# Kernel optimization log

Hardware: AMD Instinct MI355X
Metric: run time of the kernel (lower is better)

The kernel has to match this reference:

```python
import jax, jax.numpy as jnp
import numpy as np

B, T, D, H, W = 256, 512, 64, 128, 256

def _init_linear(key, out_dim, in_dim):
    lim = 1.0 / np.sqrt(in_dim)
    return jax.random.uniform(key, (out_dim, in_dim), jnp.float32, -lim, lim)

def setup_inputs():
    key = jax.random.key(0)
    ks = jax.random.split(key, 12)
    inp = {}
    inp['ts'] = jnp.arange(T, dtype=jnp.float32)
    for n, k in zip(['coeffs_d', 'coeffs_c', 'coeffs_b', 'coeffs_a'], ks[:4]):
        inp[n] = jax.random.normal(k, (B, T - 1, D), jnp.float32) * 0.05
    # initial MLP: D -> W -> W -> H (relu hidden, identity final)
    inp['i_w0'] = _init_linear(ks[4], W, D); inp['i_b0'] = jnp.zeros((W,), jnp.float32)
    inp['i_w1'] = _init_linear(ks[5], W, W); inp['i_b1'] = jnp.zeros((W,), jnp.float32)
    inp['i_w2'] = _init_linear(ks[6], H, W); inp['i_b2'] = jnp.zeros((H,), jnp.float32)
    # func MLP: H -> W -> W -> H*D (softplus hidden, tanh final)
    inp['f_w0'] = _init_linear(ks[7], W, H); inp['f_b0'] = jnp.zeros((W,), jnp.float32)
    inp['f_w1'] = _init_linear(ks[8], W, W); inp['f_b1'] = jnp.zeros((W,), jnp.float32)
    inp['f_w2'] = _init_linear(ks[9], H * D, W); inp['f_b2'] = jnp.zeros((H * D,), jnp.float32)
    # readout linear: H -> 1
    inp['l_w'] = _init_linear(ks[10], 1, H); inp['l_b'] = jnp.zeros((1,), jnp.float32)
    return inp

def reference(ts, coeffs_d, coeffs_c, coeffs_b, coeffs_a,
              i_w0, i_b0, i_w1, i_b1, i_w2, i_b2,
              f_w0, f_b0, f_w1, f_b1, f_w2, f_b2,
              l_w, l_b):
    dt = ts[1] - ts[0]
    # cubic spline value at t=ts[0]: interval 0, frac 0 -> a[0]
    x0 = coeffs_a[:, 0, :]  # [B, D]
    h = jax.nn.relu(x0 @ i_w0.T + i_b0)
    h = jax.nn.relu(h @ i_w1.T + i_b1)
    y0 = h @ i_w2.T + i_b2  # [B, H]

    def step(carry, _):
        t, y = carry
        # cubic spline derivative at t: b + 2c*frac + 3d*frac^2 on interval idx
        idx = jnp.clip(jnp.searchsorted(ts, t, side='right') - 1, 0, T - 2)
        frac = t - ts[idx]
        deriv = coeffs_b[:, idx] + 2.0 * coeffs_c[:, idx] * frac + 3.0 * coeffs_d[:, idx] * (frac * frac)  # [B, D]
        # vector field f(y): [B, H, D]
        g = jax.nn.softplus(y @ f_w0.T + f_b0)
        g = jax.nn.softplus(g @ f_w1.T + f_b1)
        f = jnp.tanh(g @ f_w2.T + f_b2).reshape(B, H, D)
        # Euler step: y1 = y + (f @ dX/dt) * dt
        y1 = y + jnp.einsum('bhd,bd->bh', f, deriv) * dt
        return (t + dt, y1), y1

    _, ys = jax.lax.scan(step, (ts[0], y0), None, length=T)
    # prediction = sigmoid(linear(ys[-1]))[0], per batch element
    return jax.nn.sigmoid(ys[-1] @ l_w.T + l_b)[:, 0]  # [B]
```

## Files before the change

kernel.cpp:

```cpp
#include <hip/hip_runtime.h>
#include <hip/hip_bf16.h>
#include <stdint.h>


#define BB 256
#define DD 64
#define HH 128
#define WW 256
#define HD 8192
#define TSTEPS 512
#define PAD_Y 152
#define PAD_G 280
#define PAD_DV 68

typedef __bf16 bf16x8 __attribute__((ext_vector_type(8)));
typedef __bf16 bf16x4 __attribute__((ext_vector_type(4)));
typedef float f32x4 __attribute__((ext_vector_type(4)));

__device__ __forceinline__ float softplus_f(float x) {
  return (x > 15.f) ? x : __logf(1.f + __expf(x));
}
__device__ __forceinline__ float tanh_f(float x) {
  float e = __expf(2.f * x);
  return 1.f - 2.f / (e + 1.f);
}

__device__ __forceinline__ void publish_y(uint32_t* slot, int idx, float val, uint32_t tag) {
  unsigned short ub = __builtin_bit_cast(unsigned short, (__bf16)val);
  __hip_atomic_store(&slot[idx], (tag << 16) | (uint32_t)ub,
                     __ATOMIC_RELAXED, __HIP_MEMORY_SCOPE_AGENT);
}

__global__ void prep_kernel(const float* __restrict__ w0, const float* __restrict__ w1,
                            const float* __restrict__ w2,
                            __bf16* __restrict__ w0b, __bf16* __restrict__ w1b,
                            __bf16* __restrict__ w2b) {
  int stride = gridDim.x * blockDim.x;
  int i0 = blockIdx.x * blockDim.x + threadIdx.x;
  for (int i = i0; i < WW * HH; i += stride) w0b[i] = (__bf16)w0[i];
  for (int i = i0; i < WW * WW; i += stride) w1b[i] = (__bf16)w1[i];
  for (int i = i0; i < HD * WW; i += stride) w2b[i] = (__bf16)w2[i];
}

__global__ __launch_bounds__(256) void init_kernel(
    const float* __restrict__ ca, const float* __restrict__ iw0, const float* __restrict__ ib0,
    const float* __restrict__ iw1, const float* __restrict__ ib1,
    const float* __restrict__ iw2, const float* __restrict__ ib2,
    float* __restrict__ y0) {
  __shared__ float x0[DD];
  __shared__ float h0[WW];
  __shared__ float h1[WW];
  int b = blockIdx.x, t = threadIdx.x;
  if (t < DD) x0[t] = ca[((size_t)b * 511) * DD + t];
  __syncthreads();
  float a = ib0[t];
  for (int d = 0; d < DD; ++d) a = fmaf(x0[d], iw0[t * DD + d], a);
  h0[t] = fmaxf(a, 0.f);
  __syncthreads();
  a = ib1[t];
  for (int d = 0; d < WW; ++d) a = fmaf(h0[d], iw1[t * WW + d], a);
  h1[t] = fmaxf(a, 0.f);
  __syncthreads();
  if (t < HH) {
    a = ib2[t];
    for (int d = 0; d < WW; ++d) a = fmaf(h1[d], iw2[t * WW + d], a);
    y0[b * HH + t] = a;
  }
}

__global__ __launch_bounds__(512, 2) void step_persist(
    const __bf16* __restrict__ w0b, const __bf16* __restrict__ w1b, const __bf16* __restrict__ w2b,
    const float* __restrict__ fb0, const float* __restrict__ fb1, const float* __restrict__ fb2,
    const float* __restrict__ cbp, const float* __restrict__ ccp, const float* __restrict__ cdp,
    float* __restrict__ yA, uint32_t* __restrict__ pk)
{
  __shared__ __align__(16) __bf16 yb[32 * PAD_Y];
  __shared__ __align__(16) __bf16 g0s[32 * PAD_G];
  __shared__ __align__(16) __bf16 g1s[32 * PAD_G];
  __shared__ __align__(16) float dv[32 * PAD_DV];
  __shared__ float pbuf[8 * 32];

  const int tid = threadIdx.x;
  const int wv = tid >> 6;
  const int l = tid & 63;
  const int l16 = l & 15;
  const int lq = l >> 4;

  const int wid = blockIdx.x;
  const int grp = wid >> 5;
  const int j = wid & 31;
  const int rb = grp * 32;
  const int c0 = j * 256;

  bf16x8 w0f[4][2], w1f[8][2], w2f[8][2];
  #pragma unroll
  for (int c = 0; c < 2; ++c) {
    int col = wv * 32 + c * 16 + l16;
    #pragma unroll
    for (int kb = 0; kb < 4; ++kb)
      w0f[kb][c] = *(const bf16x8*)&w0b[col * HH + kb * 32 + lq * 8];
    #pragma unroll
    for (int kb = 0; kb < 8; ++kb)
      w1f[kb][c] = *(const bf16x8*)&w1b[col * WW + kb * 32 + lq * 8];
    #pragma unroll
    for (int kb = 0; kb < 8; ++kb)
      w2f[kb][c] = *(const bf16x8*)&w2b[(size_t)(c0 + col) * WW + kb * 32 + lq * 8];
  }
  f32x4 b0r[2], b1r[2], b2r[2];
  #pragma unroll
  for (int c = 0; c < 2; ++c) {
    b0r[c] = *(const f32x4*)&fb0[wv * 32 + c * 16 + lq * 4];
    b1r[c] = *(const f32x4*)&fb1[wv * 32 + c * 16 + lq * 4];
    b2r[c] = *(const f32x4*)&fb2[c0 + wv * 32 + c * 16 + lq * 4];
  }

  float yreg = 0.f;
  int myidx = 0;
  if (tid < 128) {
    int r = tid & 31, hl = tid >> 5;
    myidx = (rb + r) * HH + (4 * j + hl);
    yreg = yA[myidx];
    publish_y(pk, myidx, yreg, 1u);
  }

  for (int k = 0; k < TSTEPS; ++k) {
    const uint32_t want = (uint32_t)(k + 1);
    const uint32_t* src = pk + (size_t)(k & 1) * (BB * HH);

    float dreg[4];
    {
      int kk = (k <= 510) ? k : 510;
      #pragma unroll
      for (int q = 0; q < 4; ++q) {
        int i = tid + q * 512;
        int r = i >> 6, d = i & (DD - 1);
        int off = ((rb + r) * 511 + kk) * DD + d;
        float v = cbp[off];
        if (k == 511) v += 2.f * ccp[off] + 3.f * cdp[off];
        dreg[q] = v;
      }
    }

    {
      uint32_t v[8];
      int ad[8];
      #pragma unroll
      for (int q = 0; q < 8; ++q) {
        int i = tid + q * 512;
        ad[q] = (rb + (i >> 7)) * HH + (i & (HH - 1));
        v[q] = __hip_atomic_load(&src[ad[q]], __ATOMIC_RELAXED, __HIP_MEMORY_SCOPE_AGENT);
      }
      int spins = 0;
      bool allok;
      do {
        allok = true;
        #pragma unroll
        for (int q = 0; q < 8; ++q) {
          if ((v[q] >> 16) != want) {
            allok = false;
            v[q] = __hip_atomic_load(&src[ad[q]], __ATOMIC_RELAXED, __HIP_MEMORY_SCOPE_AGENT);
          }
        }
        if (!allok) {
          __builtin_amdgcn_s_sleep(1);
          if (++spins > (1 << 20)) break;
        }
      } while (!allok);
      #pragma unroll
      for (int q = 0; q < 8; ++q) {
        int i = tid + q * 512;
        yb[(i >> 7) * PAD_Y + (i & (HH - 1))] =
            __builtin_bit_cast(__bf16, (unsigned short)(v[q] & 0xFFFFu));
      }
    }
    __syncthreads();

    {
      f32x4 acc[2][2] = {};
      #pragma unroll
      for (int kb = 0; kb < 4; ++kb) {
        bf16x8 y0 = *(const bf16x8*)&yb[l16 * PAD_Y + kb * 32 + lq * 8];
        bf16x8 y1 = *(const bf16x8*)&yb[(16 + l16) * PAD_Y + kb * 32 + lq * 8];
        #pragma unroll
        for (int c = 0; c < 2; ++c) {
          acc[c][0] = __builtin_amdgcn_mfma_f32_16x16x32_bf16(w0f[kb][c], y0, acc[c][0], 0, 0, 0);
          acc[c][1] = __builtin_amdgcn_mfma_f32_16x16x32_bf16(w0f[kb][c], y1, acc[c][1], 0, 0, 0);
        }
      }
      #pragma unroll
      for (int c = 0; c < 2; ++c)
        #pragma unroll
        for (int bt = 0; bt < 2; ++bt) {
          bf16x4 o;
          #pragma unroll
          for (int r = 0; r < 4; ++r)
            o[r] = (__bf16)softplus_f(acc[c][bt][r] + b0r[c][r]);
          *(bf16x4*)&g0s[(bt * 16 + l16) * PAD_G + wv * 32 + c * 16 + lq * 4] = o;
        }
    }
    #pragma unroll
    for (int q = 0; q < 4; ++q) {
      int i = tid + q * 512;
      dv[(i >> 6) * PAD_DV + (i & (DD - 1))] = dreg[q];
    }
    __syncthreads();

    {
      f32x4 acc[2][2] = {};
      #pragma unroll
      for (int kb = 0; kb < 8; ++kb) {
        bf16x8 a0 = *(const bf16x8*)&g0s[l16 * PAD_G + kb * 32 + lq * 8];
        bf16x8 a1 = *(const bf16x8*)&g0s[(16 + l16) * PAD_G + kb * 32 + lq * 8];
        #pragma unroll
        for (int c = 0; c < 2; ++c) {
          acc[c][0] = __builtin_amdgcn_mfma_f32_16x16x32_bf16(w1f[kb][c], a0, acc[c][0], 0, 0, 0);
          acc[c][1] = __builtin_amdgcn_mfma_f32_16x16x32_bf16(w1f[kb][c], a1, acc[c][1], 0, 0, 0);
        }
      }
      #pragma unroll
      for (int c = 0; c < 2; ++c)
        #pragma unroll
        for (int bt = 0; bt < 2; ++bt) {
          bf16x4 o;
          #pragma unroll
          for (int r = 0; r < 4; ++r)
            o[r] = (__bf16)softplus_f(acc[c][bt][r] + b1r[c][r]);
          *(bf16x4*)&g1s[(bt * 16 + l16) * PAD_G + wv * 32 + c * 16 + lq * 4] = o;
        }
    }
    __syncthreads();

    {
      f32x4 acc[2][2] = {};
      #pragma unroll
      for (int kb = 0; kb < 8; ++kb) {
        bf16x8 a0 = *(const bf16x8*)&g1s[l16 * PAD_G + kb * 32 + lq * 8];
        bf16x8 a1 = *(const bf16x8*)&g1s[(16 + l16) * PAD_G + kb * 32 + lq * 8];
        #pragma unroll
        for (int c = 0; c < 2; ++c) {
          acc[c][0] = __builtin_amdgcn_mfma_f32_16x16x32_bf16(w2f[kb][c], a0, acc[c][0], 0, 0, 0);
          acc[c][1] = __builtin_amdgcn_mfma_f32_16x16x32_bf16(w2f[kb][c], a1, acc[c][1], 0, 0, 0);
        }
      }
      #pragma unroll
      for (int bt = 0; bt < 2; ++bt) {
        float p = 0.f;
        #pragma unroll
        for (int c = 0; c < 2; ++c) {
          f32x4 dvv = *(const f32x4*)&dv[(bt * 16 + l16) * PAD_DV +
                                         (wv & 1) * 32 + c * 16 + lq * 4];
          #pragma unroll
          for (int r = 0; r < 4; ++r) {
            float f = tanh_f(acc[c][bt][r] + b2r[c][r]);
            p = fmaf(f, dvv[r], p);
          }
        }
        p += __shfl_xor(p, 16);
        p += __shfl_xor(p, 32);
        if (l < 16) pbuf[wv * 32 + bt * 16 + l] = p;
      }
    }
    __syncthreads();

    if (tid < 128) {
      int hl = tid >> 5, r = tid & 31;
      yreg += pbuf[(2 * hl) * 32 + r] + pbuf[(2 * hl + 1) * 32 + r];
      publish_y(pk + (size_t)((k + 1) & 1) * (BB * HH), myidx, yreg, (uint32_t)(k + 2));
    }
    __syncthreads();
  }

  if (tid < 128) yA[myidx] = yreg;
}

__global__ __launch_bounds__(256) void final_kernel(const float* __restrict__ y,
                                                    const float* __restrict__ lw,
                                                    const float* __restrict__ lb,
                                                    float* __restrict__ out) {
  int b = threadIdx.x;
  float a = lb[0];
  for (int h = 0; h < HH; ++h) a = fmaf(y[b * HH + h], lw[h], a);
  out[b] = 1.f / (1.f + __expf(-a));
}

extern "C" void kernel_launch(void* const* d_in, const int* in_sizes, int n_in,
                              void* d_out, int out_size, void* d_ws, size_t ws_size,
                              hipStream_t stream) {
  const float* cdp = (const float*)d_in[1];
  const float* ccp = (const float*)d_in[2];
  const float* cbp = (const float*)d_in[3];
  const float* cap = (const float*)d_in[4];
  const float* iw0 = (const float*)d_in[5];
  const float* ib0 = (const float*)d_in[6];
  const float* iw1 = (const float*)d_in[7];
  const float* ib1 = (const float*)d_in[8];
  const float* iw2 = (const float*)d_in[9];
  const float* ib2 = (const float*)d_in[10];
  const float* fw0 = (const float*)d_in[11];
  const float* fb0 = (const float*)d_in[12];
  const float* fw1 = (const float*)d_in[13];
  const float* fb1 = (const float*)d_in[14];
  const float* fw2 = (const float*)d_in[15];
  const float* fb2 = (const float*)d_in[16];
  const float* lw  = (const float*)d_in[17];
  const float* lb  = (const float*)d_in[18];

  char* ws = (char*)d_ws;
  __bf16* w0b = (__bf16*)(ws);
  __bf16* w1b = (__bf16*)(ws + 65536);
  __bf16* w2b = (__bf16*)(ws + 65536 + 131072);
  float* yA = (float*)(ws + 65536 + 131072 + 4194304);
  uint32_t* pk = (uint32_t*)(ws + 65536 + 131072 + 4194304 + 131072);

  hipMemsetAsync(pk, 0, 2 * BB * HH * sizeof(uint32_t), stream);
  prep_kernel<<<512, 256, 0, stream>>>(fw0, fw1, fw2, w0b, w1b, w2b);
  init_kernel<<<BB, 256, 0, stream>>>(cap, iw0, ib0, iw1, ib1, iw2, ib2, yA);
  step_persist<<<256, 512, 0, stream>>>(w0b, w1b, w2b, fb0, fb1, fb2,
                                        cbp, ccp, cdp, yA, pk);
  final_kernel<<<1, 256, 0, stream>>>(yA, lw, lb, (float*)d_out);

  (void)in_sizes; (void)n_in; (void)out_size; (void)ws_size;
}
```

Measured before the change: 4.053 ms.

## Split first two MLP layers onto two leader blocks per group with flag sync

Previously every one of the 32 blocks in a batch group recomputed the first two MLP layers for all 32 rows. Now two leader blocks per group each compute those layers for 16 rows, publish the second hidden activation to global memory, and signal through a per-group flag. All blocks then spin on the flags, load the shared activations and run the large third layer. Per-element tagged y values are replaced by plain float stores plus per-block flags, and spline pointers are advanced incrementally. The intent is to remove redundant layer-1/2 work and cut polling traffic. The cost is an extra global handoff and dependency on the leaders on the critical path every step, and occupancy is lowered to one block per CU.

```diff
diff --git a/kernel.cpp b/kernel.cpp
--- a/kernel.cpp
+++ b/kernel.cpp
@@ -9,6 +9,8 @@
 #define WW 256
 #define HD 8192
 #define TSTEPS 512
+#define NGRP 8
+#define GSZ 32
 #define PAD_Y 152
 #define PAD_G 280
 #define PAD_DV 68
@@ -24,11 +26,16 @@
   float e = __expf(2.f * x);
   return 1.f - 2.f / (e + 1.f);
 }
-
-__device__ __forceinline__ void publish_y(uint32_t* slot, int idx, float val, uint32_t tag) {
-  unsigned short ub = __builtin_bit_cast(unsigned short, (__bf16)val);
-  __hip_atomic_store(&slot[idx], (tag << 16) | (uint32_t)ub,
-                     __ATOMIC_RELAXED, __HIP_MEMORY_SCOPE_AGENT);
+__device__ __forceinline__ uint32_t pack_bf16x2(float a, float b) {
+  unsigned short ua = __builtin_bit_cast(unsigned short, (__bf16)a);
+  unsigned short ub = __builtin_bit_cast(unsigned short, (__bf16)b);
+  return (uint32_t)ua | ((uint32_t)ub << 16);
+}
+__device__ __forceinline__ uint32_t aload(const uint32_t* p) {
+  return __hip_atomic_load(p, __ATOMIC_RELAXED, __HIP_MEMORY_SCOPE_AGENT);
+}
+__device__ __forceinline__ void astore(uint32_t* p, uint32_t v) {
+  __hip_atomic_store(p, v, __ATOMIC_RELAXED, __HIP_MEMORY_SCOPE_AGENT);
 }
 
 __global__ void prep_kernel(const float* __restrict__ w0, const float* __restrict__ w1,
@@ -68,14 +75,15 @@
   }
 }
 
-__global__ __launch_bounds__(512, 2) void step_persist(
+__global__ __launch_bounds__(512, 1) void step_persist(
     const __bf16* __restrict__ w0b, const __bf16* __restrict__ w1b, const __bf16* __restrict__ w2b,
     const float* __restrict__ fb0, const float* __restrict__ fb1, const float* __restrict__ fb2,
     const float* __restrict__ cbp, const float* __restrict__ ccp, const float* __restrict__ cdp,
-    float* __restrict__ yA, uint32_t* __restrict__ pk)
+    float* __restrict__ yA, uint32_t* __restrict__ pky, uint32_t* __restrict__ pg,
+    uint32_t* __restrict__ yflag, uint32_t* __restrict__ gflag)
 {
-  __shared__ __align__(16) __bf16 yb[32 * PAD_Y];
-  __shared__ __align__(16) __bf16 g0s[32 * PAD_G];
+  __shared__ __align__(16) __bf16 yb[16 * PAD_Y];
+  __shared__ __align__(16) __bf16 g0s[16 * PAD_G];
   __shared__ __align__(16) __bf16 g1s[32 * PAD_G];
   __shared__ __align__(16) float dv[32 * PAD_DV];
   __shared__ float pbuf[8 * 32];
@@ -89,29 +97,31 @@
   const int wid = blockIdx.x;
   const int grp = wid >> 5;
   const int j = wid & 31;
+  const int jr = (j - 4 * grp) & 31;
+  const bool isLeader = (jr < 2);
   const int rb = grp * 32;
   const int c0 = j * 256;
 
-  bf16x8 w0f[4][2], w1f[8][2], w2f[8][2];
+  bf16x8 w2f[8][2];
+  f32x4 b2r[2];
   #pragma unroll
   for (int c = 0; c < 2; ++c) {
     int col = wv * 32 + c * 16 + l16;
     #pragma unroll
-    for (int kb = 0; kb < 4; ++kb)
-      w0f[kb][c] = *(const bf16x8*)&w0b[col * HH + kb * 32 + lq * 8];
-    #pragma unroll
-    for (int kb = 0; kb < 8; ++kb)
-      w1f[kb][c] = *(const bf16x8*)&w1b[col * WW + kb * 32 + lq * 8];
-    #pragma unroll
     for (int kb = 0; kb < 8; ++kb)
       w2f[kb][c] = *(const bf16x8*)&w2b[(size_t)(c0 + col) * WW + kb * 32 + lq * 8];
-  }
-  f32x4 b0r[2], b1r[2], b2r[2];
+    b2r[c] = *(const f32x4*)&fb2[c0 + wv * 32 + c * 16 + lq * 4];
+  }
+
+  const float* pcb[4];
+  float ex[4];
   #pragma unroll
-  for (int c = 0; c < 2; ++c) {
-    b0r[c] = *(const f32x4*)&fb0[wv * 32 + c * 16 + lq * 4];
-    b1r[c] = *(const f32x4*)&fb1[wv * 32 + c * 16 + lq * 4];
-    b2r[c] = *(const f32x4*)&fb2[c0 + wv * 32 + c * 16 + lq * 4];
+  for (int q = 0; q < 4; ++q) {
+    int i = tid + q * 512;
+    int r = i >> 6, d = i & (DD - 1);
+    size_t base = ((size_t)(rb + r) * 511) * DD + d;
+    pcb[q] = cbp + base;
+    ex[q] = 2.f * ccp[base + (size_t)510 * DD] + 3.f * cdp[base + (size_t)510 * DD];
   }
 
   float yreg = 0.f;
@@ -120,113 +130,125 @@
     int r = tid & 31, hl = tid >> 5;
     myidx = (rb + r) * HH + (4 * j + hl);
     yreg = yA[myidx];
-    publish_y(pk, myidx, yreg, 1u);
-  }
+    astore(&pky[myidx], __builtin_bit_cast(uint32_t, yreg));
+  }
+  __syncthreads();
+  if (tid == 0) astore(&yflag[grp * GSZ + j], 1u);
 
   for (int k = 0; k < TSTEPS; ++k) {
     const uint32_t want = (uint32_t)(k + 1);
-    const uint32_t* src = pk + (size_t)(k & 1) * (BB * HH);
-
-    float dreg[4];
-    {
-      int kk = (k <= 510) ? k : 510;
+
+    #pragma unroll
+    for (int q = 0; q < 4; ++q) {
+      float v = *pcb[q];
+      if (k < 510) pcb[q] += DD;
+      if (k == 511) v += ex[q];
+      int i = tid + q * 512;
+      dv[(i >> 6) * PAD_DV + (i & (DD - 1))] = v;
+    }
+
+    uint32_t* pgs = pg + (size_t)(k & 1) * (NGRP * 4096) + grp * 4096;
+
+    if (isLeader) {
+      bf16x8 w0t[4][2], w1t[8][2];
+      f32x4 b0r[2], b1r[2];
       #pragma unroll
-      for (int q = 0; q < 4; ++q) {
-        int i = tid + q * 512;
-        int r = i >> 6, d = i & (DD - 1);
-        int off = ((rb + r) * 511 + kk) * DD + d;
-        float v = cbp[off];
-        if (k == 511) v += 2.f * ccp[off] + 3.f * cdp[off];
-        dreg[q] = v;
-      }
-    }
-
-    {
-      uint32_t v[8];
-      int ad[8];
-      #pragma unroll
-      for (int q = 0; q < 8; ++q) {
-        int i = tid + q * 512;
-        ad[q] = (rb + (i >> 7)) * HH + (i & (HH - 1));
-        v[q] = __hip_atomic_load(&src[ad[q]], __ATOMIC_RELAXED, __HIP_MEMORY_SCOPE_AGENT);
-      }
-      int spins = 0;
-      bool allok;
-      do {
-        allok = true;
-        #pragma unroll
-        for (int q = 0; q < 8; ++q) {
-          if ((v[q] >> 16) != want) {
-            allok = false;
-            v[q] = __hip_atomic_load(&src[ad[q]], __ATOMIC_RELAXED, __HIP_MEMORY_SCOPE_AGENT);
-          }
-        }
-        if (!allok) {
+      for (int c = 0; c < 2; ++c) {
+        int col = wv * 32 + c * 16 + l16;
+        #pragma unroll
+        for (int kb = 0; kb < 4; ++kb)
+          w0t[kb][c] = *(const bf16x8*)&w0b[col * HH + kb * 32 + lq * 8];
+        #pragma unroll
+        for (int kb = 0; kb < 8; ++kb)
+          w1t[kb][c] = *(const bf16x8*)&w1b[col * WW + kb * 32 + lq * 8];
+        b0r[c] = *(const f32x4*)&fb0[wv * 32 + c * 16 + lq * 4];
+        b1r[c] = *(const f32x4*)&fb1[wv * 32 + c * 16 + lq * 4];
+      }
+      {
+        const uint32_t* yf = yflag + grp * GSZ + (l & 31);
+        const bool need = (l < 32);
+        int spins = 0;
+        while (true) {
+          uint32_t f = need ? aload(yf) : want;
+          if (__all(f == want)) break;
           __builtin_amdgcn_s_sleep(1);
-          if (++spins > (1 << 20)) break;
-        }
-      } while (!allok);
-      #pragma unroll
-      for (int q = 0; q < 8; ++q) {
-        int i = tid + q * 512;
-        yb[(i >> 7) * PAD_Y + (i & (HH - 1))] =
-            __builtin_bit_cast(__bf16, (unsigned short)(v[q] & 0xFFFFu));
-      }
-    }
-    __syncthreads();
-
-    {
-      f32x4 acc[2][2] = {};
-      #pragma unroll
-      for (int kb = 0; kb < 4; ++kb) {
-        bf16x8 y0 = *(const bf16x8*)&yb[l16 * PAD_Y + kb * 32 + lq * 8];
-        bf16x8 y1 = *(const bf16x8*)&yb[(16 + l16) * PAD_Y + kb * 32 + lq * 8];
+          if (++spins > (1 << 22)) break;
+        }
+      }
+      __asm__ __volatile__("" ::: "memory");
+      {
+        const uint32_t* ysl = pky + (size_t)(k & 1) * (BB * HH);
+        #pragma unroll
+        for (int q = 0; q < 4; ++q) {
+          int i = tid + q * 512;
+          int rl = i >> 7, h = i & (HH - 1);
+          uint32_t w = aload(&ysl[(rb + 16 * jr + rl) * HH + h]);
+          yb[rl * PAD_Y + h] = (__bf16)__builtin_bit_cast(float, w);
+        }
+      }
+      __syncthreads();
+      {
+        f32x4 acc[2] = {};
+        #pragma unroll
+        for (int kb = 0; kb < 4; ++kb) {
+          bf16x8 yf8 = *(const bf16x8*)&yb[l16 * PAD_Y + kb * 32 + lq * 8];
+          #pragma unroll
+          for (int c = 0; c < 2; ++c)
+            acc[c] = __builtin_amdgcn_mfma_f32_16x16x32_bf16(w0t[kb][c], yf8, acc[c], 0, 0, 0);
+        }
         #pragma unroll
         for (int c = 0; c < 2; ++c) {
-          acc[c][0] = __builtin_amdgcn_mfma_f32_16x16x32_bf16(w0f[kb][c], y0, acc[c][0], 0, 0, 0);
-          acc[c][1] = __builtin_amdgcn_mfma_f32_16x16x32_bf16(w0f[kb][c], y1, acc[c][1], 0, 0, 0);
-        }
-      }
-      #pragma unroll
-      for (int c = 0; c < 2; ++c)
-        #pragma unroll
-        for (int bt = 0; bt < 2; ++bt) {
           bf16x4 o;
           #pragma unroll
           for (int r = 0; r < 4; ++r)
-            o[r] = (__bf16)softplus_f(acc[c][bt][r] + b0r[c][r]);
-          *(bf16x4*)&g0s[(bt * 16 + l16) * PAD_G + wv * 32 + c * 16 + lq * 4] = o;
-        }
-    }
+            o[r] = (__bf16)softplus_f(acc[c][r] + b0r[c][r]);
+          *(bf16x4*)&g0s[l16 * PAD_G + wv * 32 + c * 16 + lq * 4] = o;
+        }
+      }
+      __syncthreads();
+      {
+        f32x4 acc[2] = {};
+        #pragma unroll
+        for (int kb = 0; kb < 8; ++kb) {
+          bf16x8 a8 = *(const bf16x8*)&g0s[l16 * PAD_G + kb * 32 + lq * 8];
+          #pragma unroll
+          for (int c = 0; c < 2; ++c)
+            acc[c] = __builtin_amdgcn_mfma_f32_16x16x32_bf16(w1t[kb][c], a8, acc[c], 0, 0, 0);
+        }
+        int gr = 16 * jr + l16;
+        #pragma unroll
+        for (int c = 0; c < 2; ++c) {
+          float v0 = softplus_f(acc[c][0] + b1r[c][0]);
+          float v1 = softplus_f(acc[c][1] + b1r[c][1]);
+          float v2 = softplus_f(acc[c][2] + b1r[c][2]);
+          float v3 = softplus_f(acc[c][3] + b1r[c][3]);
+          int p = wv * 16 + c * 8 + lq * 2;
+          astore(&pgs[gr * 128 + p], pack_bf16x2(v0, v1));
+          astore(&pgs[gr * 128 + p + 1], pack_bf16x2(v2, v3));
+        }
+      }
+      __syncthreads();
+      if (tid == 0) astore(&gflag[grp * 2 + jr], want);
+    }
+
+    {
+      const uint32_t* gf = gflag + grp * 2 + (l & 1);
+      const bool need = (l < 2);
+      int spins = 0;
+      while (true) {
+        uint32_t f = need ? aload(gf) : want;
+        if (__all(f == want)) break;
+        __builtin_amdgcn_s_sleep(2);
+        if (++spins > (1 << 22)) break;
+      }
+    }
+    __asm__ __volatile__("" ::: "memory");
     #pragma unroll
-    for (int q = 0; q < 4; ++q) {
+    for (int q = 0; q < 8; ++q) {
       int i = tid + q * 512;
-      dv[(i >> 6) * PAD_DV + (i & (DD - 1))] = dreg[q];
-    }
-    __syncthreads();
-
-    {
-      f32x4 acc[2][2] = {};
-      #pragma unroll
-      for (int kb = 0; kb < 8; ++kb) {
-        bf16x8 a0 = *(const bf16x8*)&g0s[l16 * PAD_G + kb * 32 + lq * 8];
-        bf16x8 a1 = *(const bf16x8*)&g0s[(16 + l16) * PAD_G + kb * 32 + lq * 8];
-        #pragma unroll
-        for (int c = 0; c < 2; ++c) {
-          acc[c][0] = __builtin_amdgcn_mfma_f32_16x16x32_bf16(w1f[kb][c], a0, acc[c][0], 0, 0, 0);
-          acc[c][1] = __builtin_amdgcn_mfma_f32_16x16x32_bf16(w1f[kb][c], a1, acc[c][1], 0, 0, 0);
-        }
-      }
-      #pragma unroll
-      for (int c = 0; c < 2; ++c)
-        #pragma unroll
-        for (int bt = 0; bt < 2; ++bt) {
-          bf16x4 o;
-          #pragma unroll
-          for (int r = 0; r < 4; ++r)
-            o[r] = (__bf16)softplus_f(acc[c][bt][r] + b1r[c][r]);
-          *(bf16x4*)&g1s[(bt * 16 + l16) * PAD_G + wv * 32 + c * 16 + lq * 4] = o;
-        }
+      int row = i >> 7, p = i & 127;
+      uint32_t w = aload(&pgs[row * 128 + p]);
+      *(uint32_t*)&g1s[row * PAD_G + 2 * p] = w;
     }
     __syncthreads();
 
@@ -265,9 +287,11 @@
     if (tid < 128) {
       int hl = tid >> 5, r = tid & 31;
       yreg += pbuf[(2 * hl) * 32 + r] + pbuf[(2 * hl + 1) * 32 + r];
-      publish_y(pk + (size_t)((k + 1) & 1) * (BB * HH), myidx, yreg, (uint32_t)(k + 2));
+      uint32_t* ydst = pky + (size_t)((k + 1) & 1) * (BB * HH);
+      astore(&ydst[myidx], __builtin_bit_cast(uint32_t, yreg));
     }
     __syncthreads();
+    if (tid == 0) astore(&yflag[grp * GSZ + j], (uint32_t)(k + 2));
   }
 
   if (tid < 128) yA[myidx] = yreg;
@@ -308,15 +332,18 @@
   char* ws = (char*)d_ws;
   __bf16* w0b = (__bf16*)(ws);
   __bf16* w1b = (__bf16*)(ws + 65536);
-  __bf16* w2b = (__bf16*)(ws + 65536 + 131072);
-  float* yA = (float*)(ws + 65536 + 131072 + 4194304);
-  uint32_t* pk = (uint32_t*)(ws + 65536 + 131072 + 4194304 + 131072);
-
-  hipMemsetAsync(pk, 0, 2 * BB * HH * sizeof(uint32_t), stream);
+  __bf16* w2b = (__bf16*)(ws + 196608);
+  float* yA = (float*)(ws + 4390912);
+  uint32_t* pky = (uint32_t*)(ws + 4521984);
+  uint32_t* pg  = (uint32_t*)(ws + 4784128);
+  uint32_t* yflag = (uint32_t*)(ws + 5046272);
+  uint32_t* gflag = (uint32_t*)(ws + 5047296);
+
+  hipMemsetAsync(yflag, 0, 2048, stream);
   prep_kernel<<<512, 256, 0, stream>>>(fw0, fw1, fw2, w0b, w1b, w2b);
   init_kernel<<<BB, 256, 0, stream>>>(cap, iw0, ib0, iw1, ib1, iw2, ib2, yA);
   step_persist<<<256, 512, 0, stream>>>(w0b, w1b, w2b, fb0, fb1, fb2,
-                                        cbp, ccp, cdp, yA, pk);
+                                        cbp, ccp, cdp, yA, pky, pg, yflag, gflag);
   final_kernel<<<1, 256, 0, stream>>>(yA, lw, lb, (float*)d_out);
 
   (void)in_sizes; (void)n_in; (void)out_size; (void)ws_size;
```

New measurement: 7.615 ms. +87.9%, slower.

## Move W2 weights to LDS, reload W0/W1 per step, load spline derivs directly

Applied to the files above, without the earlier changes.

The per-block W2 weight slice moves from registers into dynamic LDS (about 158 KB), and W0/W1 fragments are re-fetched from global/L2 each time step instead of being held in registers. This cuts register pressure. The g0/g1 buffers are merged into one reused buffer, which adds barriers between the layers. Spline derivative values are now loaded straight into MFMA-layout registers instead of being staged through LDS. The trade-off is more LDS and L2 traffic per step and extra synchronisation, in exchange for fewer VGPRs and possibly less spilling.

```diff
diff --git a/kernel.cpp b/kernel.cpp
--- a/kernel.cpp
+++ b/kernel.cpp
@@ -9,9 +9,14 @@
 #define WW 256
 #define HD 8192
 #define TSTEPS 512
-#define PAD_Y 152
-#define PAD_G 280
-#define PAD_DV 68
+#define PAD_Y 136
+#define PAD_G 264
+
+#define SM_W2   0
+#define SM_YB   131072
+#define SM_G    140288
+#define SM_PBUF 157184
+#define SM_TOT  158208
 
 typedef __bf16 bf16x8 __attribute__((ext_vector_type(8)));
 typedef __bf16 bf16x4 __attribute__((ext_vector_type(4)));
@@ -24,7 +29,6 @@
   float e = __expf(2.f * x);
   return 1.f - 2.f / (e + 1.f);
 }
-
 __device__ __forceinline__ void publish_y(uint32_t* slot, int idx, float val, uint32_t tag) {
   unsigned short ub = __builtin_bit_cast(unsigned short, (__bf16)val);
   __hip_atomic_store(&slot[idx], (tag << 16) | (uint32_t)ub,
@@ -68,17 +72,18 @@
   }
 }
 
-__global__ __launch_bounds__(512, 2) void step_persist(
+__global__ __attribute__((amdgpu_flat_work_group_size(512, 512), amdgpu_waves_per_eu(2, 2)))
+void step_persist(
     const __bf16* __restrict__ w0b, const __bf16* __restrict__ w1b, const __bf16* __restrict__ w2b,
     const float* __restrict__ fb0, const float* __restrict__ fb1, const float* __restrict__ fb2,
     const float* __restrict__ cbp, const float* __restrict__ ccp, const float* __restrict__ cdp,
     float* __restrict__ yA, uint32_t* __restrict__ pk)
 {
-  __shared__ __align__(16) __bf16 yb[32 * PAD_Y];
-  __shared__ __align__(16) __bf16 g0s[32 * PAD_G];
-  __shared__ __align__(16) __bf16 g1s[32 * PAD_G];
-  __shared__ __align__(16) float dv[32 * PAD_DV];
-  __shared__ float pbuf[8 * 32];
+  extern __shared__ __align__(16) char smem[];
+  __bf16* w2l = (__bf16*)(smem + SM_W2);
+  __bf16* yb  = (__bf16*)(smem + SM_YB);
+  __bf16* g   = (__bf16*)(smem + SM_G);
+  float* pbuf = (float*)(smem + SM_PBUF);
 
   const int tid = threadIdx.x;
   const int wv = tid >> 6;
@@ -92,20 +97,13 @@
   const int rb = grp * 32;
   const int c0 = j * 256;
 
-  bf16x8 w0f[4][2], w1f[8][2], w2f[8][2];
-  #pragma unroll
-  for (int c = 0; c < 2; ++c) {
-    int col = wv * 32 + c * 16 + l16;
-    #pragma unroll
-    for (int kb = 0; kb < 4; ++kb)
-      w0f[kb][c] = *(const bf16x8*)&w0b[col * HH + kb * 32 + lq * 8];
-    #pragma unroll
-    for (int kb = 0; kb < 8; ++kb)
-      w1f[kb][c] = *(const bf16x8*)&w1b[col * WW + kb * 32 + lq * 8];
-    #pragma unroll
-    for (int kb = 0; kb < 8; ++kb)
-      w2f[kb][c] = *(const bf16x8*)&w2b[(size_t)(c0 + col) * WW + kb * 32 + lq * 8];
-  }
+  for (int blk = tid; blk < 8192; blk += 512) {
+    int kq = blk >> 8, col = blk & 255;
+    int kb = kq >> 2, lq2 = kq & 3;
+    *(bf16x8*)&w2l[(size_t)blk * 8] =
+        *(const bf16x8*)&w2b[(size_t)(c0 + col) * WW + kb * 32 + lq2 * 8];
+  }
+
   f32x4 b0r[2], b1r[2], b2r[2];
   #pragma unroll
   for (int c = 0; c < 2; ++c) {
@@ -113,6 +111,13 @@
     b1r[c] = *(const f32x4*)&fb1[wv * 32 + c * 16 + lq * 4];
     b2r[c] = *(const f32x4*)&fb2[c0 + wv * 32 + c * 16 + lq * 4];
   }
+
+  size_t cb2[2];
+  #pragma unroll
+  for (int bt = 0; bt < 2; ++bt)
+    cb2[bt] = ((size_t)(rb + bt * 16 + l16) * 511) * DD + (wv & 1) * 32 + lq * 4;
+
+  const int w2base = lq * 2048 + (wv * 32 + l16) * 8;
 
   float yreg = 0.f;
   int myidx = 0;
@@ -122,24 +127,24 @@
     yreg = yA[myidx];
     publish_y(pk, myidx, yreg, 1u);
   }
+  __syncthreads();
 
   for (int k = 0; k < TSTEPS; ++k) {
     const uint32_t want = (uint32_t)(k + 1);
     const uint32_t* src = pk + (size_t)(k & 1) * (BB * HH);
 
-    float dreg[4];
-    {
-      int kk = (k <= 510) ? k : 510;
-      #pragma unroll
-      for (int q = 0; q < 4; ++q) {
-        int i = tid + q * 512;
-        int r = i >> 6, d = i & (DD - 1);
-        int off = ((rb + r) * 511 + kk) * DD + d;
-        float v = cbp[off];
-        if (k == 511) v += 2.f * ccp[off] + 3.f * cdp[off];
-        dreg[q] = v;
-      }
-    }
+    bf16x8 w0f[4][2], w1f[8][2];
+    #pragma unroll
+    for (int c = 0; c < 2; ++c) {
+      int col = wv * 32 + c * 16 + l16;
+      #pragma unroll
+      for (int kb = 0; kb < 4; ++kb)
+        w0f[kb][c] = *(const bf16x8*)&w0b[col * HH + kb * 32 + lq * 8];
+      #pragma unroll
+      for (int kb = 0; kb < 8; ++kb)
+        w1f[kb][c] = *(const bf16x8*)&w1b[col * WW + kb * 32 + lq * 8];
+    }
+    __asm__ __volatile__("" ::: "memory");
 
     {
       uint32_t v[8];
@@ -195,51 +200,68 @@
           #pragma unroll
           for (int r = 0; r < 4; ++r)
             o[r] = (__bf16)softplus_f(acc[c][bt][r] + b0r[c][r]);
-          *(bf16x4*)&g0s[(bt * 16 + l16) * PAD_G + wv * 32 + c * 16 + lq * 4] = o;
-        }
-    }
+          *(bf16x4*)&g[(bt * 16 + l16) * PAD_G + wv * 32 + c * 16 + lq * 4] = o;
+        }
+    }
+    __syncthreads();
+
+    f32x4 dv_[2][2];
+    {
+      size_t ko = (size_t)((k <= 510) ? k : 510) * DD;
+      #pragma unroll
+      for (int bt = 0; bt < 2; ++bt)
+        #pragma unroll
+        for (int c = 0; c < 2; ++c) {
+          size_t off = cb2[bt] + ko + c * 16;
+          dv_[bt][c] = *(const f32x4*)&cbp[off];
+          if (k == 511) {
+            f32x4 cc = *(const f32x4*)&ccp[off];
+            f32x4 dd = *(const f32x4*)&cdp[off];
+            #pragma unroll
+            for (int r = 0; r < 4; ++r)
+              dv_[bt][c][r] += 2.f * cc[r] + 3.f * dd[r];
+          }
+        }
+    }
+
+    f32x4 acc1[2][2] = {};
+    {
+      #pragma unroll
+      for (int kb = 0; kb < 8; ++kb) {
+        bf16x8 a0 = *(const bf16x8*)&g[l16 * PAD_G + kb * 32 + lq * 8];
+        bf16x8 a1 = *(const bf16x8*)&g[(16 + l16) * PAD_G + kb * 32 + lq * 8];
+        #pragma unroll
+        for (int c = 0; c < 2; ++c) {
+          acc1[c][0] = __builtin_amdgcn_mfma_f32_16x16x32_bf16(w1f[kb][c], a0, acc1[c][0], 0, 0, 0);
+          acc1[c][1] = __builtin_amdgcn_mfma_f32_16x16x32_bf16(w1f[kb][c], a1, acc1[c][1], 0, 0, 0);
+        }
+      }
+    }
+    __syncthreads();
+
     #pragma unroll
-    for (int q = 0; q < 4; ++q) {
-      int i = tid + q * 512;
-      dv[(i >> 6) * PAD_DV + (i & (DD - 1))] = dreg[q];
-    }
+    for (int c = 0; c < 2; ++c)
+      #pragma unroll
+      for (int bt = 0; bt < 2; ++bt) {
+        bf16x4 o;
+        #pragma unroll
+        for (int r = 0; r < 4; ++r)
+          o[r] = (__bf16)softplus_f(acc1[c][bt][r] + b1r[c][r]);
+        *(bf16x4*)&g[(bt * 16 + l16) * PAD_G + wv * 32 + c * 16 + lq * 4] = o;
+      }
     __syncthreads();
 
     {
       f32x4 acc[2][2] = {};
       #pragma unroll
       for (int kb = 0; kb < 8; ++kb) {
-        bf16x8 a0 = *(const bf16x8*)&g0s[l16 * PAD_G + kb * 32 + lq * 8];
-        bf16x8 a1 = *(const bf16x8*)&g0s[(16 + l16) * PAD_G + kb * 32 + lq * 8];
-        #pragma unroll
-        for (int c = 0; c < 2; ++c) {
-          acc[c][0] = __builtin_amdgcn_mfma_f32_16x16x32_bf16(w1f[kb][c], a0, acc[c][0], 0, 0, 0);
-          acc[c][1] = __builtin_amdgcn_mfma_f32_16x16x32_bf16(w1f[kb][c], a1, acc[c][1], 0, 0, 0);
-        }
-      }
-      #pragma unroll
-      for (int c = 0; c < 2; ++c)
-        #pragma unroll
-        for (int bt = 0; bt < 2; ++bt) {
-          bf16x4 o;
-          #pragma unroll
-          for (int r = 0; r < 4; ++r)
-            o[r] = (__bf16)softplus_f(acc[c][bt][r] + b1r[c][r]);
-          *(bf16x4*)&g1s[(bt * 16 + l16) * PAD_G + wv * 32 + c * 16 + lq * 4] = o;
-        }
-    }
-    __syncthreads();
-
-    {
-      f32x4 acc[2][2] = {};
-      #pragma unroll
-      for (int kb = 0; kb < 8; ++kb) {
-        bf16x8 a0 = *(const bf16x8*)&g1s[l16 * PAD_G + kb * 32 + lq * 8];
-        bf16x8 a1 = *(const bf16x8*)&g1s[(16 + l16) * PAD_G + kb * 32 + lq * 8];
-        #pragma unroll
-        for (int c = 0; c < 2; ++c) {
-          acc[c][0] = __builtin_amdgcn_mfma_f32_16x16x32_bf16(w2f[kb][c], a0, acc[c][0], 0, 0, 0);
-          acc[c][1] = __builtin_amdgcn_mfma_f32_16x16x32_bf16(w2f[kb][c], a1, acc[c][1], 0, 0, 0);
+        bf16x8 a0 = *(const bf16x8*)&g[l16 * PAD_G + kb * 32 + lq * 8];
+        bf16x8 a1 = *(const bf16x8*)&g[(16 + l16) * PAD_G + kb * 32 + lq * 8];
+        #pragma unroll
+        for (int c = 0; c < 2; ++c) {
+          bf16x8 wf = *(const bf16x8*)&w2l[w2base + kb * 8192 + c * 128];
+          acc[c][0] = __builtin_amdgcn_mfma_f32_16x16x32_bf16(wf, a0, acc[c][0], 0, 0, 0);
+          acc[c][1] = __builtin_amdgcn_mfma_f32_16x16x32_bf16(wf, a1, acc[c][1], 0, 0, 0);
         }
       }
       #pragma unroll
@@ -247,12 +269,10 @@
         float p = 0.f;
         #pragma unroll
         for (int c = 0; c < 2; ++c) {
-          f32x4 dvv = *(const f32x4*)&dv[(bt * 16 + l16) * PAD_DV +
-                                         (wv & 1) * 32 + c * 16 + lq * 4];
           #pragma unroll
           for (int r = 0; r < 4; ++r) {
             float f = tanh_f(acc[c][bt][r] + b2r[c][r]);
-            p = fmaf(f, dvv[r], p);
+            p = fmaf(f, dv_[bt][c][r], p);
           }
         }
         p += __shfl_xor(p, 16);
@@ -315,8 +335,8 @@
   hipMemsetAsync(pk, 0, 2 * BB * HH * sizeof(uint32_t), stream);
   prep_kernel<<<512, 256, 0, stream>>>(fw0, fw1, fw2, w0b, w1b, w2b);
   init_kernel<<<BB, 256, 0, stream>>>(cap, iw0, ib0, iw1, ib1, iw2, ib2, yA);
-  step_persist<<<256, 512, 0, stream>>>(w0b, w1b, w2b, fb0, fb1, fb2,
-                                        cbp, ccp, cdp, yA, pk);
+  step_persist<<<256, 512, SM_TOT, stream>>>(w0b, w1b, w2b, fb0, fb1, fb2,
+                                             cbp, ccp, cdp, yA, pk);
   final_kernel<<<1, 256, 0, stream>>>(yA, lw, lb, (float*)d_out);
 
   (void)in_sizes; (void)n_in; (void)out_size; (void)ws_size;
```

Result: slower. 4.361 ms (+7.6%).

## Remap final layer per wave to drop shared-memory reduction and barriers

Applied to the files above, without the earlier changes.

The final GEMM is reorganised so each wave owns a 16-row by one-h output tile, covering 64 columns with 4 MFMA accumulators. The dot product with the spline derivative and the Euler update then finish inside the wave and are published directly, which removes the pbuf reduction, the dv staging in shared memory and two block barriers per step. Derivative coefficients are loaded as vectors straight into registers, and the y buffer is double-buffered so the end-of-step barrier can go. The cost is that w2 is no longer held in registers and is reloaded from global memory/L2 on every step, alongside a VGPR cap attribute and smaller padding.

```diff
diff --git a/kernel.cpp b/kernel.cpp
--- a/kernel.cpp
+++ b/kernel.cpp
@@ -9,9 +9,8 @@
 #define WW 256
 #define HD 8192
 #define TSTEPS 512
-#define PAD_Y 152
-#define PAD_G 280
-#define PAD_DV 68
+#define PAD_Y 136
+#define PAD_G 264
 
 typedef __bf16 bf16x8 __attribute__((ext_vector_type(8)));
 typedef __bf16 bf16x4 __attribute__((ext_vector_type(4)));
@@ -24,7 +23,9 @@
   float e = __expf(2.f * x);
   return 1.f - 2.f / (e + 1.f);
 }
-
+__device__ __forceinline__ uint32_t aload(const uint32_t* p) {
+  return __hip_atomic_load(p, __ATOMIC_RELAXED, __HIP_MEMORY_SCOPE_AGENT);
+}
 __device__ __forceinline__ void publish_y(uint32_t* slot, int idx, float val, uint32_t tag) {
   unsigned short ub = __builtin_bit_cast(unsigned short, (__bf16)val);
   __hip_atomic_store(&slot[idx], (tag << 16) | (uint32_t)ub,
@@ -68,17 +69,19 @@
   }
 }
 
-__global__ __launch_bounds__(512, 2) void step_persist(
+__global__ __attribute__((amdgpu_flat_work_group_size(512, 512), amdgpu_waves_per_eu(2, 2)))
+#if __has_attribute(amdgpu_num_vgpr)
+__attribute__((amdgpu_num_vgpr(224)))
+#endif
+void step_persist(
     const __bf16* __restrict__ w0b, const __bf16* __restrict__ w1b, const __bf16* __restrict__ w2b,
     const float* __restrict__ fb0, const float* __restrict__ fb1, const float* __restrict__ fb2,
     const float* __restrict__ cbp, const float* __restrict__ ccp, const float* __restrict__ cdp,
     float* __restrict__ yA, uint32_t* __restrict__ pk)
 {
-  __shared__ __align__(16) __bf16 yb[32 * PAD_Y];
+  __shared__ __align__(16) __bf16 yb[2][32 * PAD_Y];
   __shared__ __align__(16) __bf16 g0s[32 * PAD_G];
   __shared__ __align__(16) __bf16 g1s[32 * PAD_G];
-  __shared__ __align__(16) float dv[32 * PAD_DV];
-  __shared__ float pbuf[8 * 32];
 
   const int tid = threadIdx.x;
   const int wv = tid >> 6;
@@ -91,34 +94,33 @@
   const int j = wid & 31;
   const int rb = grp * 32;
   const int c0 = j * 256;
-
-  bf16x8 w0f[4][2], w1f[8][2], w2f[8][2];
+  const int rt = wv >> 2;
+  const int hq = wv & 3;
+
+  bf16x8 w0f[4][2], w1f[8][2];
+  f32x4 b0r[2], b1r[2];
   #pragma unroll
-  for (int c = 0; c < 2; ++c) {
-    int col = wv * 32 + c * 16 + l16;
+  for (int cc = 0; cc < 2; ++cc) {
+    int colA = wv * 32 + cc * 16 + l16;
     #pragma unroll
     for (int kb = 0; kb < 4; ++kb)
-      w0f[kb][c] = *(const bf16x8*)&w0b[col * HH + kb * 32 + lq * 8];
+      w0f[kb][cc] = *(const bf16x8*)&w0b[colA * HH + kb * 32 + lq * 8];
     #pragma unroll
     for (int kb = 0; kb < 8; ++kb)
-      w1f[kb][c] = *(const bf16x8*)&w1b[col * WW + kb * 32 + lq * 8];
-    #pragma unroll
-    for (int kb = 0; kb < 8; ++kb)
-      w2f[kb][c] = *(const bf16x8*)&w2b[(size_t)(c0 + col) * WW + kb * 32 + lq * 8];
+      w1f[kb][cc] = *(const bf16x8*)&w1b[colA * WW + kb * 32 + lq * 8];
+    b0r[cc] = *(const f32x4*)&fb0[wv * 32 + cc * 16 + lq * 4];
+    b1r[cc] = *(const f32x4*)&fb1[wv * 32 + cc * 16 + lq * 4];
   }
-  f32x4 b0r[2], b1r[2], b2r[2];
+  f32x4 b2r[4];
   #pragma unroll
-  for (int c = 0; c < 2; ++c) {
-    b0r[c] = *(const f32x4*)&fb0[wv * 32 + c * 16 + lq * 4];
-    b1r[c] = *(const f32x4*)&fb1[wv * 32 + c * 16 + lq * 4];
-    b2r[c] = *(const f32x4*)&fb2[c0 + wv * 32 + c * 16 + lq * 4];
-  }
-
+  for (int c = 0; c < 4; ++c)
+    b2r[c] = *(const f32x4*)&fb2[c0 + hq * 64 + c * 16 + lq * 4];
+
+  const size_t dvbase = ((size_t)(rb + rt * 16 + l16) * 511) * DD + lq * 4;
+
+  const int myidx = (rb + rt * 16 + l16) * HH + (4 * j + hq);
   float yreg = 0.f;
-  int myidx = 0;
-  if (tid < 128) {
-    int r = tid & 31, hl = tid >> 5;
-    myidx = (rb + r) * HH + (4 * j + hl);
+  if (l < 16) {
     yreg = yA[myidx];
     publish_y(pk, myidx, yreg, 1u);
   }
@@ -126,18 +128,21 @@
   for (int k = 0; k < TSTEPS; ++k) {
     const uint32_t want = (uint32_t)(k + 1);
     const uint32_t* src = pk + (size_t)(k & 1) * (BB * HH);
-
-    float dreg[4];
-    {
-      int kk = (k <= 510) ? k : 510;
-      #pragma unroll
-      for (int q = 0; q < 4; ++q) {
-        int i = tid + q * 512;
-        int r = i >> 6, d = i & (DD - 1);
-        int off = ((rb + r) * 511 + kk) * DD + d;
-        float v = cbp[off];
-        if (k == 511) v += 2.f * ccp[off] + 3.f * cdp[off];
-        dreg[q] = v;
+    __bf16* ybk = yb[k & 1];
+
+    f32x4 dvv[4];
+    {
+      size_t ko = dvbase + (size_t)((k <= 510) ? k : 510) * DD;
+      #pragma unroll
+      for (int c = 0; c < 4; ++c) dvv[c] = *(const f32x4*)&cbp[ko + c * 16];
+      if (k == 511) {
+        #pragma unroll
+        for (int c = 0; c < 4; ++c) {
+          f32x4 cc = *(const f32x4*)&ccp[ko + c * 16];
+          f32x4 dd = *(const f32x4*)&cdp[ko + c * 16];
+          #pragma unroll
+          for (int r = 0; r < 4; ++r) dvv[c][r] += 2.f * cc[r] + 3.f * dd[r];
+        }
       }
     }
 
@@ -147,8 +152,8 @@
       #pragma unroll
       for (int q = 0; q < 8; ++q) {
         int i = tid + q * 512;
-        ad[q] = (rb + (i >> 7)) * HH + (i & (HH - 1));
-        v[q] = __hip_atomic_load(&src[ad[q]], __ATOMIC_RELAXED, __HIP_MEMORY_SCOPE_AGENT);
+        ad[q] = (rb + (i >> 7)) * HH + (i & 127);
+        v[q] = aload(&src[ad[q]]);
       }
       int spins = 0;
       bool allok;
@@ -158,7 +163,7 @@
         for (int q = 0; q < 8; ++q) {
           if ((v[q] >> 16) != want) {
             allok = false;
-            v[q] = __hip_atomic_load(&src[ad[q]], __ATOMIC_RELAXED, __HIP_MEMORY_SCOPE_AGENT);
+            v[q] = aload(&src[ad[q]]);
           }
         }
         if (!allok) {
@@ -169,7 +174,7 @@
       #pragma unroll
       for (int q = 0; q < 8; ++q) {
         int i = tid + q * 512;
-        yb[(i >> 7) * PAD_Y + (i & (HH - 1))] =
+        ybk[(i >> 7) * PAD_Y + (i & 127)] =
             __builtin_bit_cast(__bf16, (unsigned short)(v[q] & 0xFFFFu));
       }
     }
@@ -179,29 +184,24 @@
       f32x4 acc[2][2] = {};
       #pragma unroll
       for (int kb = 0; kb < 4; ++kb) {
-        bf16x8 y0 = *(const bf16x8*)&yb[l16 * PAD_Y + kb * 32 + lq * 8];
-        bf16x8 y1 = *(const bf16x8*)&yb[(16 + l16) * PAD_Y + kb * 32 + lq * 8];
-        #pragma unroll
-        for (int c = 0; c < 2; ++c) {
-          acc[c][0] = __builtin_amdgcn_mfma_f32_16x16x32_bf16(w0f[kb][c], y0, acc[c][0], 0, 0, 0);
-          acc[c][1] = __builtin_amdgcn_mfma_f32_16x16x32_bf16(w0f[kb][c], y1, acc[c][1], 0, 0, 0);
-        }
-      }
-      #pragma unroll
-      for (int c = 0; c < 2; ++c)
+        bf16x8 y0 = *(const bf16x8*)&ybk[l16 * PAD_Y + kb * 32 + lq * 8];
+        bf16x8 y1 = *(const bf16x8*)&ybk[(16 + l16) * PAD_Y + kb * 32 + lq * 8];
+        #pragma unroll
+        for (int cc = 0; cc < 2; ++cc) {
+          acc[cc][0] = __builtin_amdgcn_mfma_f32_16x16x32_bf16(w0f[kb][cc], y0, acc[cc][0], 0, 0, 0);
+          acc[cc][1] = __builtin_amdgcn_mfma_f32_16x16x32_bf16(w0f[kb][cc], y1, acc[cc][1], 0, 0, 0);
+        }
+      }
+      #pragma unroll
+      for (int cc = 0; cc < 2; ++cc)
         #pragma unroll
         for (int bt = 0; bt < 2; ++bt) {
           bf16x4 o;
           #pragma unroll
           for (int r = 0; r < 4; ++r)
-            o[r] = (__bf16)softplus_f(acc[c][bt][r] + b0r[c][r]);
-          *(bf16x4*)&g0s[(bt * 16 + l16) * PAD_G + wv * 32 + c * 16 + lq * 4] = o;
-        }
-    }
-    #pragma unroll
-    for (int q = 0; q < 4; ++q) {
-      int i = tid + q * 512;
-      dv[(i >> 6) * PAD_DV + (i & (DD - 1))] = dreg[q];
+            o[r] = (__bf16)softplus_f(acc[cc][bt][r] + b0r[cc][r]);
+          *(bf16x4*)&g0s[(bt * 16 + l16) * PAD_G + wv * 32 + cc * 16 + lq * 4] = o;
+        }
     }
     __syncthreads();
 
@@ -212,65 +212,54 @@
         bf16x8 a0 = *(const bf16x8*)&g0s[l16 * PAD_G + kb * 32 + lq * 8];
         bf16x8 a1 = *(const bf16x8*)&g0s[(16 + l16) * PAD_G + kb * 32 + lq * 8];
         #pragma unroll
-        for (int c = 0; c < 2; ++c) {
-          acc[c][0] = __builtin_amdgcn_mfma_f32_16x16x32_bf16(w1f[kb][c], a0, acc[c][0], 0, 0, 0);
-          acc[c][1] = __builtin_amdgcn_mfma_f32_16x16x32_bf16(w1f[kb][c], a1, acc[c][1], 0, 0, 0);
-        }
-      }
-      #pragma unroll
-      for (int c = 0; c < 2; ++c)
+        for (int cc = 0; cc < 2; ++cc) {
+          acc[cc][0] = __builtin_amdgcn_mfma_f32_16x16x32_bf16(w1f[kb][cc], a0, acc[cc][0], 0, 0, 0);
+          acc[cc][1] = __builtin_amdgcn_mfma_f32_16x16x32_bf16(w1f[kb][cc], a1, acc[cc][1], 0, 0, 0);
+        }
+      }
+      #pragma unroll
+      for (int cc = 0; cc < 2; ++cc)
         #pragma unroll
         for (int bt = 0; bt < 2; ++bt) {
           bf16x4 o;
           #pragma unroll
           for (int r = 0; r < 4; ++r)
-            o[r] = (__bf16)softplus_f(acc[c][bt][r] + b1r[c][r]);
-          *(bf16x4*)&g1s[(bt * 16 + l16) * PAD_G + wv * 32 + c * 16 + lq * 4] = o;
+            o[r] = (__bf16)softplus_f(acc[cc][bt][r] + b1r[cc][r]);
+          *(bf16x4*)&g1s[(bt * 16 + l16) * PAD_G + wv * 32 + cc * 16 + lq * 4] = o;
         }
     }
     __syncthreads();
 
     {
-      f32x4 acc[2][2] = {};
+      f32x4 acc[4] = {};
       #pragma unroll
       for (int kb = 0; kb < 8; ++kb) {
-        bf16x8 a0 = *(const bf16x8*)&g1s[l16 * PAD_G + kb * 32 + lq * 8];
-        bf16x8 a1 = *(const bf16x8*)&g1s[(16 + l16) * PAD_G + kb * 32 + lq * 8];
-        #pragma unroll
-        for (int c = 0; c < 2; ++c) {
-          acc[c][0] = __builtin_amdgcn_mfma_f32_16x16x32_bf16(w2f[kb][c], a0, acc[c][0], 0, 0, 0);
-          acc[c][1] = __builtin_amdgcn_mfma_f32_16x16x32_bf16(w2f[kb][c], a1, acc[c][1], 0, 0, 0);
-        }
-      }
-      #pragma unroll
-      for (int bt = 0; bt < 2; ++bt) {
-        float p = 0.f;
-        #pragma unroll
-        for (int c = 0; c < 2; ++c) {
-          f32x4 dvv = *(const f32x4*)&dv[(bt * 16 + l16) * PAD_DV +
-                                         (wv & 1) * 32 + c * 16 + lq * 4];
-          #pragma unroll
-          for (int r = 0; r < 4; ++r) {
-            float f = tanh_f(acc[c][bt][r] + b2r[c][r]);
-            p = fmaf(f, dvv[r], p);
-          }
-        }
-        p += __shfl_xor(p, 16);
-        p += __shfl_xor(p, 32);
-        if (l < 16) pbuf[wv * 32 + bt * 16 + l] = p;
-      }
-    }
-    __syncthreads();
-
-    if (tid < 128) {
-      int hl = tid >> 5, r = tid & 31;
-      yreg += pbuf[(2 * hl) * 32 + r] + pbuf[(2 * hl + 1) * 32 + r];
-      publish_y(pk + (size_t)((k + 1) & 1) * (BB * HH), myidx, yreg, (uint32_t)(k + 2));
-    }
-    __syncthreads();
+        bf16x8 a0 = *(const bf16x8*)&g1s[(rt * 16 + l16) * PAD_G + kb * 32 + lq * 8];
+        #pragma unroll
+        for (int c = 0; c < 4; ++c) {
+          bf16x8 wf = *(const bf16x8*)&w2b[(size_t)(c0 + hq * 64 + c * 16 + l16) * WW +
+                                           kb * 32 + lq * 8];
+          acc[c] = __builtin_amdgcn_mfma_f32_16x16x32_bf16(wf, a0, acc[c], 0, 0, 0);
+        }
+      }
+      float pp = 0.f;
+      #pragma unroll
+      for (int c = 0; c < 4; ++c)
+        #pragma unroll
+        for (int r = 0; r < 4; ++r) {
+          float f = tanh_f(acc[c][r] + b2r[c][r]);
+          pp = fmaf(f, dvv[c][r], pp);
+        }
+      pp += __shfl_xor(pp, 16);
+      pp += __shfl_xor(pp, 32);
+      if (l < 16) {
+        yreg += pp;
+        publish_y(pk + (size_t)((k + 1) & 1) * (BB * HH), myidx, yreg, (uint32_t)(k + 2));
+      }
+    }
   }
 
-  if (tid < 128) yA[myidx] = yreg;
+  if (l < 16) yA[myidx] = yreg;
 }
 
 __global__ __launch_bounds__(256) void final_kernel(const float* __restrict__ y,
```

New measurement: 10.59 ms. +161.3%, slower.
